# Kernel optimization log

Measured on AMD Instinct MI355X. Metric: run time of the kernel, lower is better.

Reference implementation:

```python
import jax, jax.numpy as jnp
import numpy as np

N = 50000      # nodes
E = 500000     # edges (avg in-degree 10)
DIN = 256      # in_dim
D = 128        # out_dim


def setup_inputs() -> dict:
    key = jax.random.key(0)
    ks = jax.random.split(key, 8)
    x = jax.random.normal(ks[0], (N, DIN), jnp.float32)
    efeat = jax.random.normal(ks[1], (E, D), jnp.float32)
    att_node = jax.random.uniform(ks[2], (N,), jnp.float32)
    att_edge = jax.random.uniform(ks[3], (E,), jnp.float32)
    src = jax.random.randint(ks[4], (E,), 0, N, dtype=jnp.int32)
    # every node gets in-degree >= 1 (DGL skips zero-in-degree nodes in reduce)
    dst = (jnp.arange(E, dtype=jnp.int32) % N)
    Wn = jax.random.normal(ks[5], (D, DIN), jnp.float32) * (1.0 / np.sqrt(DIN))
    bn = jnp.zeros((D,), jnp.float32)
    Wa = jax.random.normal(ks[6], (D, 3 * D), jnp.float32) * (1.0 / np.sqrt(3 * D))
    ba = jnp.zeros((D,), jnp.float32)
    return {"x": x, "efeat": efeat, "att_node": att_node, "att_edge": att_edge,
            "src": src, "dst": dst, "Wn": Wn, "bn": bn, "Wa": Wa, "ba": ba}


def reference(x, efeat, att_node, att_edge, src, dst, Wn, bn, Wa, ba):
    # apply_node: node feat = node_fc(feat)                      [N, D]
    h = x @ Wn.T + bn
    # message: z1 = att_src * src_feat, z2 = att_e * edge_feat   [E, 2D]
    z1 = att_node[src][:, None] * h[src]
    z2 = att_edge[:, None] * efeat
    msg = jnp.concatenate([z1, z2], axis=1)
    # reduce: scatter-sum messages to dst nodes                  [N, 2D]
    agg = jax.ops.segment_sum(msg, dst, num_segments=N)
    # relu(apply_fc_node(cat[msg_sum, h])) scaled by node att    [N, D]
    r = jax.nn.relu(jnp.concatenate([agg, h], axis=1) @ Wa.T + ba)
    return att_node[:, None] * r
```

## Files before the change

### kernel.cpp

```cpp
#include <hip/hip_runtime.h>

#define NN 50000
#define EE 500000
#define KEDGE 10

typedef unsigned short u16;
typedef unsigned int u32;
using f32x4  = __attribute__((ext_vector_type(4))) float;
using bf16x8 = __attribute__((ext_vector_type(8))) short;

#define OF_WFT   0
#define OF_BF    32768
#define OF_WABT  33024
#define OF_G     41216
#define OF_PRE   (OF_G + NN * 128)
#define OF_AGG2  (OF_PRE + NN * 128)

__device__ __forceinline__ u16 f2bf(float f) {
    u32 u = __float_as_uint(f);
    u32 r = (u + 0x7fffu + ((u >> 16) & 1u)) >> 16;
    return (u16)r;
}
__device__ __forceinline__ float bf2f(u16 u) {
    return __uint_as_float(((u32)u) << 16);
}

__global__ void k_fuse_w(const float* __restrict__ Wn, const float* __restrict__ bn,
                         const float* __restrict__ Wa, u16* __restrict__ WfT,
                         float* __restrict__ bf) {
    int jp = blockIdx.x;
    if (jp < 256) {
        int jj  = jp & 127;
        int off = (jp < 128) ? 0 : 256;
        int k = threadIdx.x;
        float acc = 0.f;
        for (int i = 0; i < 128; ++i)
            acc = fmaf(Wn[i * 256 + k], Wa[jj * 384 + off + i], acc);
        WfT[jp * 256 + k] = f2bf(acc);
    } else {
        int j = threadIdx.x;
        int jj  = j & 127;
        int off = (j < 128) ? 0 : 256;
        float acc = 0.f;
        for (int i = 0; i < 128; ++i)
            acc = fmaf(bn[i], Wa[jj * 384 + off + i], acc);
        bf[j] = acc;
    }
}

__global__ void k_prep_wab(const float* __restrict__ Wa, u16* __restrict__ WaBfT) {
    int j = blockIdx.x;
    int k = threadIdx.x;
    WaBfT[j * 128 + k] = f2bf(Wa[j * 384 + 128 + k]);
}

__global__ __launch_bounds__(256) void k_gemm_G(const float* __restrict__ x,
                                                const u16* __restrict__ WfT,
                                                const float* __restrict__ bf,
                                                u16* __restrict__ G) {
    __shared__ __align__(16) u16 As[128 * 64];
    __shared__ __align__(16) u16 Bs[128 * 64];
    const int t  = threadIdx.x;
    const int m0 = blockIdx.x * 128;
    const int j0 = blockIdx.y * 128;
    const int w  = t >> 6, l = t & 63;
    const int wm = w >> 1, wn = w & 1;
    const int lr = l & 15, lg = l >> 4;
    f32x4 acc[4][4];
#pragma unroll
    for (int a = 0; a < 4; ++a)
#pragma unroll
        for (int b = 0; b < 4; ++b) { acc[a][b][0]=0.f; acc[a][b][1]=0.f; acc[a][b][2]=0.f; acc[a][b][3]=0.f; }

    for (int kt = 0; kt < 256; kt += 64) {
#pragma unroll
        for (int p = 0; p < 8; ++p) {
            int f   = t + p * 256;
            int row = f >> 4, c4 = f & 15;
            int gm  = m0 + row;
            float4 v = make_float4(0.f, 0.f, 0.f, 0.f);
            if (gm < NN) v = *(const float4*)(x + (long)gm * 256 + kt + c4 * 4);
            u32 lo = (u32)f2bf(v.x) | ((u32)f2bf(v.y) << 16);
            u32 hi = (u32)f2bf(v.z) | ((u32)f2bf(v.w) << 16);
            int byte = (row * 128 + c4 * 8) ^ ((row & 7) << 4);
            *(uint2*)((char*)As + byte) = make_uint2(lo, hi);
        }
#pragma unroll
        for (int p = 0; p < 4; ++p) {
            int f   = t + p * 256;
            int row = f >> 3, sl = f & 7;
            uint4 v = *(const uint4*)(WfT + (long)(j0 + row) * 256 + kt + sl * 8);
            int byte = (row * 128 + sl * 16) ^ ((row & 7) << 4);
            *(uint4*)((char*)Bs + byte) = v;
        }
        __syncthreads();
#pragma unroll
        for (int kk = 0; kk < 2; ++kk) {
            bf16x8 av[4], bv[4];
#pragma unroll
            for (int a = 0; a < 4; ++a) {
                int row = wm * 64 + a * 16 + lr;
                int byte = (row * 128 + kk * 64 + lg * 16) ^ ((row & 7) << 4);
                av[a] = *(bf16x8*)((char*)As + byte);
            }
#pragma unroll
            for (int b = 0; b < 4; ++b) {
                int row = wn * 64 + b * 16 + lr;
                int byte = (row * 128 + kk * 64 + lg * 16) ^ ((row & 7) << 4);
                bv[b] = *(bf16x8*)((char*)Bs + byte);
            }
#pragma unroll
            for (int a = 0; a < 4; ++a)
#pragma unroll
                for (int b = 0; b < 4; ++b)
                    acc[a][b] = __builtin_amdgcn_mfma_f32_16x16x32_bf16(av[a], bv[b], acc[a][b], 0, 0, 0);
        }
        __syncthreads();
    }
#pragma unroll
    for (int b = 0; b < 4; ++b) {
        int n = j0 + wn * 64 + b * 16 + lr;
        float bias = bf[n];
#pragma unroll
        for (int a = 0; a < 4; ++a) {
            int mbase = m0 + wm * 64 + a * 16 + lg * 4;
#pragma unroll
            for (int r = 0; r < 4; ++r) {
                int m = mbase + r;
                if (m < NN) G[(long)m * 256 + n] = f2bf(acc[a][b][r] + bias);
            }
        }
    }
}

__global__ __launch_bounds__(256) void k_gather(const u16* __restrict__ G,
                                                const float* __restrict__ efeat,
                                                const float* __restrict__ att_node,
                                                const float* __restrict__ att_edge,
                                                const int* __restrict__ src,
                                                float* __restrict__ pre,
                                                u16* __restrict__ agg2) {
    __shared__ int   sS[320];
    __shared__ float sA[320];
    __shared__ float sE[320];
    const int t  = threadIdx.x;
    const int n0 = blockIdx.x * 32;
    for (int i = t; i < 320; i += 256) {
        int m = i / 10;
        int k = i - m * 10;
        int n = n0 + m;
        int s = 0; float a = 0.f, ev = 0.f;
        if (n < NN) {
            int e = n + k * NN;
            s  = src[e];
            a  = att_node[s];
            ev = att_edge[e];
        }
        sS[i] = s; sA[i] = a; sE[i] = ev;
    }
    __syncthreads();
    const int j    = t & 127;
    const int half = t >> 7;
    if (half == 0) {
#pragma unroll 1
        for (int m = 0; m < 32; ++m) {
            int n = n0 + m;
            if (n >= NN) break;
            float acc = 0.f;
#pragma unroll
            for (int k = 0; k < KEDGE; ++k) {
                int i = m * 10 + k;
                acc = fmaf(sA[i], bf2f(G[(long)sS[i] * 256 + j]), acc);
            }
            pre[(long)n * 128 + j] = acc + bf2f(G[(long)n * 256 + 128 + j]);
        }
    } else {
#pragma unroll 1
        for (int m = 0; m < 32; ++m) {
            int n = n0 + m;
            if (n >= NN) break;
            float acc = 0.f;
#pragma unroll
            for (int k = 0; k < KEDGE; ++k) {
                acc = fmaf(sE[m * 10 + k], efeat[((long)(n + k * NN)) * 128 + j], acc);
            }
            agg2[(long)n * 128 + j] = f2bf(acc);
        }
    }
}

__global__ __launch_bounds__(256) void k_gemm_out(const u16* __restrict__ agg2,
                                                  const u16* __restrict__ WaBfT,
                                                  const float* __restrict__ pre,
                                                  const float* __restrict__ att_node,
                                                  const float* __restrict__ ba,
                                                  float* __restrict__ out) {
    __shared__ __align__(16) u16 As[128 * 64];
    __shared__ __align__(16) u16 Bs[128 * 64];
    const int t  = threadIdx.x;
    const int m0 = blockIdx.x * 128;
    const int w  = t >> 6, l = t & 63;
    const int wm = w >> 1, wn = w & 1;
    const int lr = l & 15, lg = l >> 4;
    f32x4 acc[4][4];
#pragma unroll
    for (int a = 0; a < 4; ++a)
#pragma unroll
        for (int b = 0; b < 4; ++b) { acc[a][b][0]=0.f; acc[a][b][1]=0.f; acc[a][b][2]=0.f; acc[a][b][3]=0.f; }

    for (int kt = 0; kt < 128; kt += 64) {
#pragma unroll
        for (int p = 0; p < 4; ++p) {
            int f   = t + p * 256;
            int row = f >> 3, sl = f & 7;
            int gm  = m0 + row;
            uint4 v = make_uint4(0u, 0u, 0u, 0u);
            if (gm < NN) v = *(const uint4*)(agg2 + (long)gm * 128 + kt + sl * 8);
            int byte = (row * 128 + sl * 16) ^ ((row & 7) << 4);
            *(uint4*)((char*)As + byte) = v;
        }
#pragma unroll
        for (int p = 0; p < 4; ++p) {
            int f   = t + p * 256;
            int row = f >> 3, sl = f & 7;
            uint4 v = *(const uint4*)(WaBfT + (long)row * 128 + kt + sl * 8);
            int byte = (row * 128 + sl * 16) ^ ((row & 7) << 4);
            *(uint4*)((char*)Bs + byte) = v;
        }
        __syncthreads();
#pragma unroll
        for (int kk = 0; kk < 2; ++kk) {
            bf16x8 av[4], bv[4];
#pragma unroll
            for (int a = 0; a < 4; ++a) {
                int row = wm * 64 + a * 16 + lr;
                int byte = (row * 128 + kk * 64 + lg * 16) ^ ((row & 7) << 4);
                av[a] = *(bf16x8*)((char*)As + byte);
            }
#pragma unroll
            for (int b = 0; b < 4; ++b) {
                int row = wn * 64 + b * 16 + lr;
                int byte = (row * 128 + kk * 64 + lg * 16) ^ ((row & 7) << 4);
                bv[b] = *(bf16x8*)((char*)Bs + byte);
            }
#pragma unroll
            for (int a = 0; a < 4; ++a)
#pragma unroll
                for (int b = 0; b < 4; ++b)
                    acc[a][b] = __builtin_amdgcn_mfma_f32_16x16x32_bf16(av[a], bv[b], acc[a][b], 0, 0, 0);
        }
        __syncthreads();
    }
#pragma unroll
    for (int a = 0; a < 4; ++a) {
        int mbase = m0 + wm * 64 + a * 16 + lg * 4;
#pragma unroll
        for (int r = 0; r < 4; ++r) {
            int m = mbase + r;
            if (m < NN) {
                float av = att_node[m];
#pragma unroll
                for (int b = 0; b < 4; ++b) {
                    int n = wn * 64 + b * 16 + lr;
                    float val = acc[a][b][r] + pre[(long)m * 128 + n] + ba[n];
                    out[(long)m * 128 + n] = av * fmaxf(val, 0.f);
                }
            }
        }
    }
}

extern "C" void kernel_launch(void* const* d_in, const int* in_sizes, int n_in,
                              void* d_out, int out_size, void* d_ws, size_t ws_size,
                              hipStream_t stream) {
    const float* x        = (const float*)d_in[0];
    const float* efeat    = (const float*)d_in[1];
    const float* att_node = (const float*)d_in[2];
    const float* att_edge = (const float*)d_in[3];
    const int*   src      = (const int*)d_in[4];
    const float* Wn       = (const float*)d_in[6];
    const float* bn       = (const float*)d_in[7];
    const float* Wa       = (const float*)d_in[8];
    const float* ba       = (const float*)d_in[9];
    float* out = (float*)d_out;

    float* ws    = (float*)d_ws;
    u16*   WfT   = (u16*)(ws + OF_WFT);
    float* bf    = ws + OF_BF;
    u16*   WaBfT = (u16*)(ws + OF_WABT);
    u16*   G     = (u16*)(ws + OF_G);
    float* pre   = ws + OF_PRE;
    u16*   agg2  = (u16*)(ws + OF_AGG2);

    hipLaunchKernelGGL(k_fuse_w, dim3(257), dim3(256), 0, stream, Wn, bn, Wa, WfT, bf);
    hipLaunchKernelGGL(k_prep_wab, dim3(128), dim3(128), 0, stream, Wa, WaBfT);
    hipLaunchKernelGGL(k_gemm_G, dim3(391, 2), dim3(256), 0, stream, x, WfT, bf, G);
    hipLaunchKernelGGL(k_gather, dim3(1563), dim3(256), 0, stream, G, efeat, att_node,
                       att_edge, src, pre, agg2);
    hipLaunchKernelGGL(k_gemm_out, dim3(391), dim3(256), 0, stream, agg2, WaBfT, pre,
                       att_node, ba, out);
}
```

Before: 160.7 us.

## Fuse gather and output GEMM into one kernel, dropping pre/agg2 round trips

Merges the edge/node gather kernel and the output GEMM into a single kernel that handles 128 nodes per block. The efeat aggregation goes straight into LDS as bf16 for the MFMA, and the gathered src contribution is staged in LDS as fp32 for the epilogue. This removes the global write and read of the intermediate pre and agg2 buffers and one launch. In exchange each block uses about 80 KB of LDS, which limits occupancy, and only 391 blocks run the memory-bound gather with wider float4/uint2 loads. It also swaps the hand-written bf16 conversion for the library one and adds multiple accumulators to the weight-fusion kernel.

```diff
diff --git a/kernel.cpp b/kernel.cpp
--- a/kernel.cpp
+++ b/kernel.cpp
@@ -1,4 +1,5 @@
 #include <hip/hip_runtime.h>
+#include <hip/hip_bf16.h>
 
 #define NN 50000
 #define EE 500000
@@ -13,17 +14,15 @@
 #define OF_BF    32768
 #define OF_WABT  33024
 #define OF_G     41216
-#define OF_PRE   (OF_G + NN * 128)
-#define OF_AGG2  (OF_PRE + NN * 128)
-
-__device__ __forceinline__ u16 f2bf(float f) {
-    u32 u = __float_as_uint(f);
-    u32 r = (u + 0x7fffu + ((u >> 16) & 1u)) >> 16;
-    return (u16)r;
-}
-__device__ __forceinline__ float bf2f(u16 u) {
-    return __uint_as_float(((u32)u) << 16);
-}
+
+__device__ __forceinline__ u16 f2bfc(float f) {
+    return __bfloat16_as_ushort(__float2bfloat16(f));
+}
+__device__ __forceinline__ u32 pk2(float a, float b) {
+    return (u32)f2bfc(a) | ((u32)f2bfc(b) << 16);
+}
+__device__ __forceinline__ float bflo(u32 g) { return __uint_as_float(g << 16); }
+__device__ __forceinline__ float bfhi(u32 g) { return __uint_as_float(g & 0xffff0000u); }
 
 __global__ void k_fuse_w(const float* __restrict__ Wn, const float* __restrict__ bn,
                          const float* __restrict__ Wa, u16* __restrict__ WfT,
@@ -33,10 +32,14 @@
         int jj  = jp & 127;
         int off = (jp < 128) ? 0 : 256;
         int k = threadIdx.x;
-        float acc = 0.f;
-        for (int i = 0; i < 128; ++i)
-            acc = fmaf(Wn[i * 256 + k], Wa[jj * 384 + off + i], acc);
-        WfT[jp * 256 + k] = f2bf(acc);
+        float a0 = 0.f, a1 = 0.f, a2 = 0.f, a3 = 0.f;
+        for (int i = 0; i < 128; i += 4) {
+            a0 = fmaf(Wn[(i + 0) * 256 + k], Wa[jj * 384 + off + i + 0], a0);
+            a1 = fmaf(Wn[(i + 1) * 256 + k], Wa[jj * 384 + off + i + 1], a1);
+            a2 = fmaf(Wn[(i + 2) * 256 + k], Wa[jj * 384 + off + i + 2], a2);
+            a3 = fmaf(Wn[(i + 3) * 256 + k], Wa[jj * 384 + off + i + 3], a3);
+        }
+        WfT[jp * 256 + k] = f2bfc((a0 + a1) + (a2 + a3));
     } else {
         int j = threadIdx.x;
         int jj  = j & 127;
@@ -51,7 +54,7 @@
 __global__ void k_prep_wab(const float* __restrict__ Wa, u16* __restrict__ WaBfT) {
     int j = blockIdx.x;
     int k = threadIdx.x;
-    WaBfT[j * 128 + k] = f2bf(Wa[j * 384 + 128 + k]);
+    WaBfT[j * 128 + k] = f2bfc(Wa[j * 384 + 128 + k]);
 }
 
 __global__ __launch_bounds__(256) void k_gemm_G(const float* __restrict__ x,
@@ -80,10 +83,8 @@
             int gm  = m0 + row;
             float4 v = make_float4(0.f, 0.f, 0.f, 0.f);
             if (gm < NN) v = *(const float4*)(x + (long)gm * 256 + kt + c4 * 4);
-            u32 lo = (u32)f2bf(v.x) | ((u32)f2bf(v.y) << 16);
-            u32 hi = (u32)f2bf(v.z) | ((u32)f2bf(v.w) << 16);
             int byte = (row * 128 + c4 * 8) ^ ((row & 7) << 4);
-            *(uint2*)((char*)As + byte) = make_uint2(lo, hi);
+            *(uint2*)((char*)As + byte) = make_uint2(pk2(v.x, v.y), pk2(v.z, v.w));
         }
 #pragma unroll
         for (int p = 0; p < 4; ++p) {
@@ -127,27 +128,36 @@
 #pragma unroll
             for (int r = 0; r < 4; ++r) {
                 int m = mbase + r;
-                if (m < NN) G[(long)m * 256 + n] = f2bf(acc[a][b][r] + bias);
-            }
-        }
-    }
-}
-
-__global__ __launch_bounds__(256) void k_gather(const u16* __restrict__ G,
-                                                const float* __restrict__ efeat,
-                                                const float* __restrict__ att_node,
-                                                const float* __restrict__ att_edge,
-                                                const int* __restrict__ src,
-                                                float* __restrict__ pre,
-                                                u16* __restrict__ agg2) {
-    __shared__ int   sS[320];
-    __shared__ float sA[320];
-    __shared__ float sE[320];
+                if (m < NN) G[(long)m * 256 + n] = f2bfc(acc[a][b][r] + bias);
+            }
+        }
+    }
+}
+
+__global__ __launch_bounds__(256) void k_fused_out(const u16* __restrict__ G,
+                                                   const float* __restrict__ efeat,
+                                                   const float* __restrict__ att_node,
+                                                   const float* __restrict__ att_edge,
+                                                   const int* __restrict__ src,
+                                                   const u16* __restrict__ WaBfT,
+                                                   const float* __restrict__ ba,
+                                                   float* __restrict__ out) {
+    __shared__ __align__(16) char smem[80896];
+    char*  AsB = smem;
+    char*  BsB = smem + 32768;
+    char*  PB  = smem;
+    int*   sS  = (int*)(smem + 65536);
+    float* sA  = (float*)(smem + 70656);
+    float* sE  = (float*)(smem + 75776);
+
     const int t  = threadIdx.x;
-    const int n0 = blockIdx.x * 32;
-    for (int i = t; i < 320; i += 256) {
-        int m = i / 10;
-        int k = i - m * 10;
+    const int n0 = blockIdx.x * 128;
+    const int w  = t >> 6, l = t & 63;
+    const int wm = w >> 1, wn = w & 1;
+    const int lr = l & 15, lg = l >> 4;
+
+    for (int i = t; i < 1280; i += 256) {
+        int k = i >> 7, m = i & 127;
         int n = n0 + m;
         int s = 0; float a = 0.f, ev = 0.f;
         if (n < NN) {
@@ -158,112 +168,111 @@
         }
         sS[i] = s; sA[i] = a; sE[i] = ev;
     }
+#pragma unroll
+    for (int p = 0; p < 8; ++p) {
+        int f   = t + p * 256;
+        int row = f >> 4, sl = f & 15;
+        uint4 v = *(const uint4*)(WaBfT + row * 128 + sl * 8);
+        int byte = (row * 256 + sl * 16) ^ ((row & 7) << 4);
+        *(uint4*)(BsB + byte) = v;
+    }
     __syncthreads();
-    const int j    = t & 127;
-    const int half = t >> 7;
-    if (half == 0) {
+
+    {
+        const int jq = t & 31;
+        const int mr = t >> 5;
+#pragma unroll 2
+        for (int p = 0; p < 16; ++p) {
+            int m = mr + p * 8;
+            int n = n0 + m;
+            float4 acc4 = make_float4(0.f, 0.f, 0.f, 0.f);
+            if (n < NN) {
+#pragma unroll
+                for (int k = 0; k < KEDGE; ++k) {
+                    float aE = sE[k * 128 + m];
+                    float4 v = *(const float4*)(efeat + (long)(n + k * NN) * 128 + jq * 4);
+                    acc4.x = fmaf(aE, v.x, acc4.x);
+                    acc4.y = fmaf(aE, v.y, acc4.y);
+                    acc4.z = fmaf(aE, v.z, acc4.z);
+                    acc4.w = fmaf(aE, v.w, acc4.w);
+                }
+            }
+            int byte = (m * 256 + jq * 8) ^ ((m & 7) << 4);
+            *(uint2*)(AsB + byte) = make_uint2(pk2(acc4.x, acc4.y), pk2(acc4.z, acc4.w));
+        }
+    }
+    __syncthreads();
+
+    f32x4 acc[4][4];
+#pragma unroll
+    for (int a = 0; a < 4; ++a)
+#pragma unroll
+        for (int b = 0; b < 4; ++b) { acc[a][b][0]=0.f; acc[a][b][1]=0.f; acc[a][b][2]=0.f; acc[a][b][3]=0.f; }
+#pragma unroll
+    for (int kk = 0; kk < 4; ++kk) {
+        bf16x8 av[4], bv[4];
+#pragma unroll
+        for (int a = 0; a < 4; ++a) {
+            int row = wm * 64 + a * 16 + lr;
+            int byte = (row * 256 + kk * 64 + lg * 16) ^ ((row & 7) << 4);
+            av[a] = *(bf16x8*)(AsB + byte);
+        }
+#pragma unroll
+        for (int b = 0; b < 4; ++b) {
+            int row = wn * 64 + b * 16 + lr;
+            int byte = (row * 256 + kk * 64 + lg * 16) ^ ((row & 7) << 4);
+            bv[b] = *(bf16x8*)(BsB + byte);
+        }
+#pragma unroll
+        for (int a = 0; a < 4; ++a)
+#pragma unroll
+            for (int b = 0; b < 4; ++b)
+                acc[a][b] = __builtin_amdgcn_mfma_f32_16x16x32_bf16(av[a], bv[b], acc[a][b], 0, 0, 0);
+    }
+    __syncthreads();
+
+    {
+        const int jq = t & 31;
+        const int mr = t >> 5;
 #pragma unroll 1
-        for (int m = 0; m < 32; ++m) {
+        for (int p = 0; p < 16; ++p) {
+            int m = mr + p * 8;
             int n = n0 + m;
-            if (n >= NN) break;
-            float acc = 0.f;
-#pragma unroll
-            for (int k = 0; k < KEDGE; ++k) {
-                int i = m * 10 + k;
-                acc = fmaf(sA[i], bf2f(G[(long)sS[i] * 256 + j]), acc);
-            }
-            pre[(long)n * 128 + j] = acc + bf2f(G[(long)n * 256 + 128 + j]);
-        }
-    } else {
-#pragma unroll 1
-        for (int m = 0; m < 32; ++m) {
-            int n = n0 + m;
-            if (n >= NN) break;
-            float acc = 0.f;
-#pragma unroll
-            for (int k = 0; k < KEDGE; ++k) {
-                acc = fmaf(sE[m * 10 + k], efeat[((long)(n + k * NN)) * 128 + j], acc);
-            }
-            agg2[(long)n * 128 + j] = f2bf(acc);
-        }
-    }
-}
-
-__global__ __launch_bounds__(256) void k_gemm_out(const u16* __restrict__ agg2,
-                                                  const u16* __restrict__ WaBfT,
-                                                  const float* __restrict__ pre,
-                                                  const float* __restrict__ att_node,
-                                                  const float* __restrict__ ba,
-                                                  float* __restrict__ out) {
-    __shared__ __align__(16) u16 As[128 * 64];
-    __shared__ __align__(16) u16 Bs[128 * 64];
-    const int t  = threadIdx.x;
-    const int m0 = blockIdx.x * 128;
-    const int w  = t >> 6, l = t & 63;
-    const int wm = w >> 1, wn = w & 1;
-    const int lr = l & 15, lg = l >> 4;
-    f32x4 acc[4][4];
-#pragma unroll
-    for (int a = 0; a < 4; ++a)
-#pragma unroll
-        for (int b = 0; b < 4; ++b) { acc[a][b][0]=0.f; acc[a][b][1]=0.f; acc[a][b][2]=0.f; acc[a][b][3]=0.f; }
-
-    for (int kt = 0; kt < 128; kt += 64) {
-#pragma unroll
-        for (int p = 0; p < 4; ++p) {
-            int f   = t + p * 256;
-            int row = f >> 3, sl = f & 7;
-            int gm  = m0 + row;
-            uint4 v = make_uint4(0u, 0u, 0u, 0u);
-            if (gm < NN) v = *(const uint4*)(agg2 + (long)gm * 128 + kt + sl * 8);
-            int byte = (row * 128 + sl * 16) ^ ((row & 7) << 4);
-            *(uint4*)((char*)As + byte) = v;
-        }
-#pragma unroll
-        for (int p = 0; p < 4; ++p) {
-            int f   = t + p * 256;
-            int row = f >> 3, sl = f & 7;
-            uint4 v = *(const uint4*)(WaBfT + (long)row * 128 + kt + sl * 8);
-            int byte = (row * 128 + sl * 16) ^ ((row & 7) << 4);
-            *(uint4*)((char*)Bs + byte) = v;
-        }
-        __syncthreads();
-#pragma unroll
-        for (int kk = 0; kk < 2; ++kk) {
-            bf16x8 av[4], bv[4];
-#pragma unroll
-            for (int a = 0; a < 4; ++a) {
-                int row = wm * 64 + a * 16 + lr;
-                int byte = (row * 128 + kk * 64 + lg * 16) ^ ((row & 7) << 4);
-                av[a] = *(bf16x8*)((char*)As + byte);
-            }
-#pragma unroll
-            for (int b = 0; b < 4; ++b) {
-                int row = wn * 64 + b * 16 + lr;
-                int byte = (row * 128 + kk * 64 + lg * 16) ^ ((row & 7) << 4);
-                bv[b] = *(bf16x8*)((char*)Bs + byte);
-            }
-#pragma unroll
-            for (int a = 0; a < 4; ++a)
-#pragma unroll
-                for (int b = 0; b < 4; ++b)
-                    acc[a][b] = __builtin_amdgcn_mfma_f32_16x16x32_bf16(av[a], bv[b], acc[a][b], 0, 0, 0);
-        }
-        __syncthreads();
-    }
+            float4 acc4 = make_float4(0.f, 0.f, 0.f, 0.f);
+            if (n < NN) {
+                uint2 g3 = *(const uint2*)(G + (long)n * 256 + 128 + jq * 4);
+                acc4.x = bflo(g3.x); acc4.y = bfhi(g3.x);
+                acc4.z = bflo(g3.y); acc4.w = bfhi(g3.y);
+#pragma unroll
+                for (int k = 0; k < KEDGE; ++k) {
+                    float aS = sA[k * 128 + m];
+                    uint2 g = *(const uint2*)(G + (long)sS[k * 128 + m] * 256 + jq * 4);
+                    acc4.x = fmaf(aS, bflo(g.x), acc4.x);
+                    acc4.y = fmaf(aS, bfhi(g.x), acc4.y);
+                    acc4.z = fmaf(aS, bflo(g.y), acc4.z);
+                    acc4.w = fmaf(aS, bfhi(g.y), acc4.w);
+                }
+            }
+            int byte = (m * 512 + jq * 16) ^ ((m & 7) << 4);
+            *(float4*)(PB + byte) = acc4;
+        }
+    }
+    __syncthreads();
+
 #pragma unroll
     for (int a = 0; a < 4; ++a) {
-        int mbase = m0 + wm * 64 + a * 16 + lg * 4;
 #pragma unroll
         for (int r = 0; r < 4; ++r) {
-            int m = mbase + r;
-            if (m < NN) {
-                float av = att_node[m];
+            int m  = wm * 64 + a * 16 + lg * 4 + r;
+            int gm = n0 + m;
+            if (gm < NN) {
+                float attn = att_node[gm];
 #pragma unroll
                 for (int b = 0; b < 4; ++b) {
                     int n = wn * 64 + b * 16 + lr;
-                    float val = acc[a][b][r] + pre[(long)m * 128 + n] + ba[n];
-                    out[(long)m * 128 + n] = av * fmaxf(val, 0.f);
+                    float pv = *(const float*)(PB + ((m * 512 + n * 4) ^ ((m & 7) << 4)));
+                    float val = acc[a][b][r] + pv + ba[n];
+                    out[(long)gm * 128 + n] = attn * fmaxf(val, 0.f);
                 }
             }
         }
@@ -289,14 +298,10 @@
     float* bf    = ws + OF_BF;
     u16*   WaBfT = (u16*)(ws + OF_WABT);
     u16*   G     = (u16*)(ws + OF_G);
-    float* pre   = ws + OF_PRE;
-    u16*   agg2  = (u16*)(ws + OF_AGG2);
 
     hipLaunchKernelGGL(k_fuse_w, dim3(257), dim3(256), 0, stream, Wn, bn, Wa, WfT, bf);
     hipLaunchKernelGGL(k_prep_wab, dim3(128), dim3(128), 0, stream, Wa, WaBfT);
     hipLaunchKernelGGL(k_gemm_G, dim3(391, 2), dim3(256), 0, stream, x, WfT, bf, G);
-    hipLaunchKernelGGL(k_gather, dim3(1563), dim3(256), 0, stream, G, efeat, att_node,
-                       att_edge, src, pre, agg2);
-    hipLaunchKernelGGL(k_gemm_out, dim3(391), dim3(256), 0, stream, agg2, WaBfT, pre,
-                       att_node, ba, out);
-}
+    hipLaunchKernelGGL(k_fused_out, dim3(391), dim3(256), 0, stream, G, efeat, att_node,
+                       att_edge, src, WaBfT, ba, out);
+}
```

Result: faster. 140.1 us (-12.8%).
